# Kernel optimization log

Measured on AMD Instinct MI355X. Metric: run time of the kernel, lower is better.

The kernel has to match this reference:

```python
import jax, jax.numpy as jnp
import numpy as np

N, E = 25000, 400000
NIN, NOUT, HID = 32, 32, 128


def setup_inputs() -> dict:
    key = jax.random.key(0)
    ks = jax.random.split(key, 8)
    s = lambda d: 1.0 / np.sqrt(d)
    return {
        "x": jax.random.normal(ks[0], (N, NIN), jnp.float32),
        "edge_index": jax.random.randint(ks[1], (2, E), 0, N, jnp.int64),
        "edge_attr": jax.random.normal(ks[2], (E, NIN), jnp.float32),
        # edge-MLP: Linear(NIN,HID) -> ReLU -> Linear(HID, NIN*NOUT)
        "w1": jax.random.normal(ks[3], (NIN, HID), jnp.float32) * s(NIN),
        "b1": jnp.zeros((HID,), jnp.float32),
        "w2": jax.random.normal(ks[4], (HID, NIN * NOUT), jnp.float32) * s(HID),
        "b2": jnp.zeros((NIN * NOUT,), jnp.float32),
        # NNConv root weight and bias
        "root": jax.random.normal(ks[5], (NIN, NOUT), jnp.float32) * s(NIN),
        "bias": jnp.zeros((NOUT,), jnp.float32),
    }


def reference(x, edge_index, edge_attr, w1, b1, w2, b2, root, bias):
    src, dst = edge_index[0], edge_index[1]
    # per-edge weight matrices from edge-attr MLP: [E, NIN, NOUT]
    h = jax.nn.relu(edge_attr @ w1 + b1)
    W = (h @ w2 + b2).reshape(-1, NIN, NOUT)
    # gather source features, per-edge small matmul: [E, NOUT]
    msg = jnp.einsum("ei,eio->eo", x[src], W)
    # scatter-add to target nodes (PyG default aggr='add')
    agg = jax.ops.segment_sum(msg, dst, num_segments=N)
    # root/self transform + bias
    return agg + x @ root + bias
```

## Files before the change

### kernel.cpp

```cpp
#include <hip/hip_runtime.h>
#include <hip/hip_fp16.h>


#define NN 25000
#define EE 400000

typedef _Float16 f16x8 __attribute__((ext_vector_type(8)));
typedef float    f32x16 __attribute__((ext_vector_type(16)));

__device__ __forceinline__ void async16(const void* g, void* l) {
    __builtin_amdgcn_global_load_lds(
        (const __attribute__((address_space(1))) unsigned int*)g,
        (__attribute__((address_space(3))) unsigned int*)l, 16, 0, 0);
}

__global__ __launch_bounds__(256) void prep_kernel(
    const float* __restrict__ w1, const float* __restrict__ w2,
    const float* __restrict__ b2,
    _Float16* __restrict__ w2p, _Float16* __restrict__ w1p, _Float16* __restrict__ b2p,
    float4* __restrict__ part4, int nzero4)
{
    int b = blockIdx.x;
    if (b < 532) {
        int t = b * 256 + threadIdx.x;
        if (t < 131072) {
            int j = t & 7, lane = (t >> 3) & 63, ih = (t >> 9) & 1, c = t >> 10;
            w2p[t] = (_Float16)w2[c * 1024 + (ih * 16 + ((lane >> 5) << 3) + j) * 32 + (lane & 31)];
        } else if (t < 135168) {
            int u = t - 131072;
            int j = u & 7, lane = (u >> 3) & 63, kk = (u >> 9) & 1, r = u >> 10;
            w1p[u] = (_Float16)w1[(kk * 16 + ((lane >> 5) << 3) + j) * 128 + r * 32 + (lane & 31)];
        } else {
            int u = t - 135168;
            int j = u & 7, lane = (u >> 3) & 63, ih = u >> 9;
            b2p[u] = (_Float16)b2[(ih * 16 + ((lane >> 5) << 3) + j) * 32 + (lane & 31)];
        }
    } else {
        int z = (b - 532) * 256 + threadIdx.x;
        if (z < nzero4) part4[z] = make_float4(0.f, 0.f, 0.f, 0.f);
    }
}

__global__ __launch_bounds__(256) void final_kernel(
    const float* __restrict__ x, const float* __restrict__ root,
    const float* __restrict__ bias, const float* __restrict__ part,
    int ncopies, float* __restrict__ out)
{
    int gid = blockIdx.x * 256 + threadIdx.x;
    int n = gid >> 5, o = gid & 31;
    float acc = bias[o];
    const float* xr = x + (n << 5);
#pragma unroll
    for (int i = 0; i < 32; ++i)
        acc = fmaf(xr[i], root[(i << 5) + o], acc);
    for (int c = 0; c < ncopies; ++c) acc += part[(size_t)c * 800000 + gid];
    out[gid] = acc;
}

__global__ __launch_bounds__(256, 5) void edge_kernel(
    const float*    __restrict__ x,
    const int*      __restrict__ ei,
    const float*    __restrict__ ea,
    const float*    __restrict__ b1,
    const _Float16* __restrict__ w2p,
    const _Float16* __restrict__ w1p,
    const _Float16* __restrict__ b2p,
    float* __restrict__ outp, int copyMask)
{
    __shared__ __align__(16) _Float16 w2c[2][4096];
    __shared__ unsigned short hTq[4][16][32][2];

    const int t    = threadIdx.x;
    const int w    = t >> 6;
    const int lane = t & 63;
    const int l    = lane & 31;
    const int half = lane >> 5;

    const int  ebraw = blockIdx.x * 256 + w * 64;
    const bool live  = (ebraw + 64) <= EE;
    const int  ebw   = live ? ebraw : (EE - 64);

    float* __restrict__ myout = outp + (size_t)(blockIdx.x & copyMask) * 800000;

    union u8h { f16x8 v; __half2 h2[4]; };

    const char* w2g = (const char*)w2p;
    auto issueChunk = [&](int cc, int buf) {
#pragma unroll
        for (int s = 0; s < 2; ++s) {
            const int slot = s * 256 + w * 64;
            async16(w2g + (size_t)cc * 8192 + (size_t)(slot + lane) * 16,
                    (void*)&w2c[buf][slot * 8]);
        }
    };
    issueChunk(0, 0);
    issueChunk(1, 1);

    u8h eaf[2][2];
#pragma unroll
    for (int g = 0; g < 2; ++g)
#pragma unroll
        for (int kk = 0; kk < 2; ++kk) {
            const float* p = ea + (ebw + g * 32 + l) * 32 + kk * 16 + half * 8;
            float4 a0 = *(const float4*)p;
            float4 a1 = *(const float4*)(p + 4);
            eaf[g][kk].h2[0] = __float22half2_rn(make_float2(a0.x, a0.y));
            eaf[g][kk].h2[1] = __float22half2_rn(make_float2(a0.z, a0.w));
            eaf[g][kk].h2[2] = __float22half2_rn(make_float2(a1.x, a1.y));
            eaf[g][kk].h2[3] = __float22half2_rn(make_float2(a1.z, a1.w));
        }

    __half2 xs0[8], xs1[8];
    {
        int s0 = ei[ebw + l], s1 = ei[ebw + 32 + l];
#pragma unroll
        for (int ih = 0; ih < 2; ++ih) {
            float4 a0 = *(const float4*)(x + s0 * 32 + ih * 16 + half * 8);
            float4 a1 = *(const float4*)(x + s0 * 32 + ih * 16 + half * 8 + 4);
            xs0[ih*4+0] = __float22half2_rn(make_float2(a0.x, a0.y));
            xs0[ih*4+1] = __float22half2_rn(make_float2(a0.z, a0.w));
            xs0[ih*4+2] = __float22half2_rn(make_float2(a1.x, a1.y));
            xs0[ih*4+3] = __float22half2_rn(make_float2(a1.z, a1.w));
            float4 c0 = *(const float4*)(x + s1 * 32 + ih * 16 + half * 8);
            float4 c1 = *(const float4*)(x + s1 * 32 + ih * 16 + half * 8 + 4);
            xs1[ih*4+0] = __float22half2_rn(make_float2(c0.x, c0.y));
            xs1[ih*4+1] = __float22half2_rn(make_float2(c0.z, c0.w));
            xs1[ih*4+2] = __float22half2_rn(make_float2(c1.x, c1.y));
            xs1[ih*4+3] = __float22half2_rn(make_float2(c1.z, c1.w));
        }
    }

    f32x16 acc0, acc1;
#pragma unroll
    for (int i = 0; i < 16; ++i) { acc0[i] = 0.f; acc1[i] = 0.f; }

    unsigned held[8];

    auto phase1 = [&](int r) {
        f16x8 w1f0 = *(const f16x8*)(w1p + ((r * 2 + 0) * 64 + lane) * 8);
        f16x8 w1f1 = *(const f16x8*)(w1p + ((r * 2 + 1) * 64 + lane) * 8);
#pragma unroll
        for (int g = 0; g < 2; ++g) {
            f32x16 h;
#pragma unroll
            for (int i = 0; i < 16; ++i) h[i] = 0.f;
            h = __builtin_amdgcn_mfma_f32_32x32x16_f16(w1f0, eaf[g][0].v, h, 0, 0, 0);
            h = __builtin_amdgcn_mfma_f32_32x32x16_f16(w1f1, eaf[g][1].v, h, 0, 0, 0);
#pragma unroll
            for (int i = 0; i < 16; ++i) {
                int row = (i & 3) + ((i >> 2) << 3) + (half << 2);
                float hv = fmaxf(h[i] + b1[r * 32 + row], 0.f);
                unsigned short us = __half_as_ushort(__float2half(hv));
                if (i < 8) {
                    hTq[w][row][l][g] = us;
                } else {
                    int j = i - 8;
                    if (g == 0) held[j] = us;
                    else        held[j] |= (unsigned)us << 16;
                }
            }
        }
    };

    auto flushHeld = [&]() {
#pragma unroll
        for (int j = 0; j < 8; ++j) {
            int slot = (j & 3) + ((j >> 2) << 3) + (half << 2);
            *(unsigned*)&hTq[w][slot][l][0] = held[j];
        }
    };

    auto compute = [&](int cc, const _Float16* RB) {
#pragma unroll
        for (int cl = 0; cl < 4; ++cl) {
            unsigned u = *(const unsigned*)&hTq[w][((cc & 3) << 2) + cl][l][0];
            __half2 hp = *reinterpret_cast<const __half2*>(&u);
            __half2 h0 = __half2half2(__low2half(hp));
            __half2 h1 = __half2half2(__high2half(hp));
#pragma unroll
            for (int ih = 0; ih < 2; ++ih) {
                f16x8 bfr = *(const f16x8*)(RB + (((cl << 1) + ih) * 64 + lane) * 8);
                u8h A;
#pragma unroll
                for (int p = 0; p < 4; ++p)
                    A.h2[p] = __hmul2(h0, xs0[ih * 4 + p]);
                acc0 = __builtin_amdgcn_mfma_f32_32x32x16_f16(A.v, bfr, acc0, 0, 0, 0);
#pragma unroll
                for (int p = 0; p < 4; ++p)
                    A.h2[p] = __hmul2(h1, xs1[ih * 4 + p]);
                acc1 = __builtin_amdgcn_mfma_f32_32x32x16_f16(A.v, bfr, acc1, 0, 0, 0);
            }
        }
    };

    phase1(0);
    __syncthreads();

#pragma unroll 1
    for (int r = 0; r < 4; ++r) {
        if (r > 0) phase1(r);
#pragma unroll
        for (int q = 0; q < 8; ++q) {
            const int cc = r * 8 + q;
            if (q == 4) flushHeld();
            compute(cc, w2c[q & 1]);
            __syncthreads();
            if (cc + 2 < 32) issueChunk(cc + 2, q & 1);
        }
    }

#pragma unroll
    for (int ih = 0; ih < 2; ++ih) {
        f16x8 bfr = *(const f16x8*)(b2p + (ih * 64 + lane) * 8);
        u8h A;
#pragma unroll
        for (int p = 0; p < 4; ++p) A.h2[p] = xs0[ih * 4 + p];
        acc0 = __builtin_amdgcn_mfma_f32_32x32x16_f16(A.v, bfr, acc0, 0, 0, 0);
#pragma unroll
        for (int p = 0; p < 4; ++p) A.h2[p] = xs1[ih * 4 + p];
        acc1 = __builtin_amdgcn_mfma_f32_32x32x16_f16(A.v, bfr, acc1, 0, 0, 0);
    }

    if (live) {
#pragma unroll
        for (int i = 0; i < 16; ++i) {
            int el = (i & 3) + ((i >> 2) << 3) + (half << 2);
            atomicAdd(myout + ei[EE + ebw +      el] * 32 + l, acc0[i]);
            atomicAdd(myout + ei[EE + ebw + 32 + el] * 32 + l, acc1[i]);
        }
    }
}

extern "C" void kernel_launch(void* const* d_in, const int* in_sizes, int n_in,
                              void* d_out, int out_size, void* d_ws, size_t ws_size,
                              hipStream_t stream) {
    const float* x    = (const float*)d_in[0];
    const int*   ei   = (const int*)  d_in[1];
    const float* ea   = (const float*)d_in[2];
    const float* w1   = (const float*)d_in[3];
    const float* b1   = (const float*)d_in[4];
    const float* w2   = (const float*)d_in[5];
    const float* b2   = (const float*)d_in[6];
    const float* root = (const float*)d_in[7];
    const float* bias = (const float*)d_in[8];
    float* out = (float*)d_out;

    _Float16* w2p = (_Float16*)d_ws;
    _Float16* w1p = (_Float16*)((char*)d_ws + 262144);
    _Float16* b2p = (_Float16*)((char*)d_ws + 270336);
    const size_t partOff = 272384;
    const size_t one = 800000ull * sizeof(float);
    size_t avail = (ws_size > partOff) ? ws_size - partOff : 0;
    int nc = 0;
    for (int c = 8; c >= 1; c >>= 1)
        if ((size_t)c * one <= avail) { nc = c; break; }

    float* part = (float*)((char*)d_ws + partOff);
    if (nc > 0) {
        int nzero4 = nc * 200000;
        int zb = (nzero4 + 255) / 256;
        prep_kernel<<<532 + zb, 256, 0, stream>>>(w1, w2, b2, w2p, w1p, b2p,
                                                  (float4*)part, nzero4);
        edge_kernel<<<(EE + 255) / 256, 256, 0, stream>>>(x, ei, ea, b1, w2p, w1p, b2p,
                                                          part, nc - 1);
        final_kernel<<<(NN * 32) / 256, 256, 0, stream>>>(x, root, bias, part, nc, out);
    } else {
        prep_kernel<<<532, 256, 0, stream>>>(w1, w2, b2, w2p, w1p, b2p, (float4*)part, 0);
        final_kernel<<<(NN * 32) / 256, 256, 0, stream>>>(x, root, bias, part, 0, out);
        edge_kernel<<<(EE + 255) / 256, 256, 0, stream>>>(x, ei, ea, b1, w2p, w1p, b2p,
                                                          out, 0);
    }
}
```

Baseline: 257.9 us.

## Stream w2 fragments directly into registers instead of LDS double buffer

```diff
diff --git a/kernel.cpp b/kernel.cpp
--- a/kernel.cpp
+++ b/kernel.cpp
@@ -7,12 +7,6 @@
 
 typedef _Float16 f16x8 __attribute__((ext_vector_type(8)));
 typedef float    f32x16 __attribute__((ext_vector_type(16)));
-
-__device__ __forceinline__ void async16(const void* g, void* l) {
-    __builtin_amdgcn_global_load_lds(
-        (const __attribute__((address_space(1))) unsigned int*)g,
-        (__attribute__((address_space(3))) unsigned int*)l, 16, 0, 0);
-}
 
 __global__ __launch_bounds__(256) void prep_kernel(
     const float* __restrict__ w1, const float* __restrict__ w2,
@@ -57,7 +51,7 @@
     out[gid] = acc;
 }
 
-__global__ __launch_bounds__(256, 5) void edge_kernel(
+__global__ __launch_bounds__(256, 3) void edge_kernel(
     const float*    __restrict__ x,
     const int*      __restrict__ ei,
     const float*    __restrict__ ea,
@@ -67,7 +61,6 @@
     const _Float16* __restrict__ b2p,
     float* __restrict__ outp, int copyMask)
 {
-    __shared__ __align__(16) _Float16 w2c[2][4096];
     __shared__ unsigned short hTq[4][16][32][2];
 
     const int t    = threadIdx.x;
@@ -84,17 +77,16 @@
 
     union u8h { f16x8 v; __half2 h2[4]; };
 
-    const char* w2g = (const char*)w2p;
-    auto issueChunk = [&](int cc, int buf) {
-#pragma unroll
-        for (int s = 0; s < 2; ++s) {
-            const int slot = s * 256 + w * 64;
-            async16(w2g + (size_t)cc * 8192 + (size_t)(slot + lane) * 16,
-                    (void*)&w2c[buf][slot * 8]);
-        }
-    };
-    issueChunk(0, 0);
-    issueChunk(1, 1);
+    const f16x8* __restrict__ w2f = (const f16x8*)w2p;
+
+    f16x8 B0[4], B1[4];
+    auto loadHalf = [&](int hc, f16x8 (&B)[4]) {
+        const f16x8* p = w2f + (size_t)hc * 256 + lane;
+#pragma unroll
+        for (int fi = 0; fi < 4; ++fi) B[fi] = p[fi * 64];
+    };
+    loadHalf(0, B0);
+    loadHalf(1, B1);
 
     u8h eaf[2][2];
 #pragma unroll
@@ -170,16 +162,17 @@
         }
     };
 
-    auto compute = [&](int cc, const _Float16* RB) {
-#pragma unroll
-        for (int cl = 0; cl < 4; ++cl) {
-            unsigned u = *(const unsigned*)&hTq[w][((cc & 3) << 2) + cl][l][0];
+    auto computeHalf = [&](int q4, int hh, const f16x8 (&B)[4]) {
+#pragma unroll
+        for (int c2 = 0; c2 < 2; ++c2) {
+            const int cl = hh * 2 + c2;
+            unsigned u = *(const unsigned*)&hTq[w][(q4 << 2) + cl][l][0];
             __half2 hp = *reinterpret_cast<const __half2*>(&u);
             __half2 h0 = __half2half2(__low2half(hp));
             __half2 h1 = __half2half2(__high2half(hp));
 #pragma unroll
             for (int ih = 0; ih < 2; ++ih) {
-                f16x8 bfr = *(const f16x8*)(RB + (((cl << 1) + ih) * 64 + lane) * 8);
+                f16x8 bfr = B[c2 * 2 + ih];
                 u8h A;
 #pragma unroll
                 for (int p = 0; p < 4; ++p)
@@ -194,8 +187,6 @@
     };
 
     phase1(0);
-    __syncthreads();
-
 #pragma unroll 1
     for (int r = 0; r < 4; ++r) {
         if (r > 0) phase1(r);
@@ -203,9 +194,10 @@
         for (int q = 0; q < 8; ++q) {
             const int cc = r * 8 + q;
             if (q == 4) flushHeld();
-            compute(cc, w2c[q & 1]);
-            __syncthreads();
-            if (cc + 2 < 32) issueChunk(cc + 2, q & 1);
+            computeHalf(q & 3, 0, B0);
+            if (cc < 31) loadHalf(cc * 2 + 2, B0);
+            computeHalf(q & 3, 1, B1);
+            if (cc < 31) loadHalf(cc * 2 + 3, B1);
         }
     }
 
```

Result: faster. 227.8 us (-11.7%).
